# Performance work log

Hardware: AMD Instinct MI355X
Metric: run time of the kernel (lower is better)

Reference implementation:

```python
import jax, jax.numpy as jnp
import numpy as np
from jax.scipy.ndimage import map_coordinates


def _so3_exp(w):
    # Rodrigues formula, small-angle safe. w: [B,3] -> [B,3,3]
    th = jnp.linalg.norm(w, axis=-1)
    small = th < 1e-6
    ths = jnp.where(small, 1.0, th)
    A = jnp.where(small, 1.0 - th * th / 6.0, jnp.sin(ths) / ths)
    Bc = jnp.where(small, 0.5 - th * th / 24.0, (1.0 - jnp.cos(ths)) / (ths * ths))
    wx, wy, wz = w[..., 0], w[..., 1], w[..., 2]
    z = jnp.zeros_like(wx)
    K = jnp.stack([
        jnp.stack([z, -wz, wy], -1),
        jnp.stack([wz, z, -wx], -1),
        jnp.stack([-wy, wx, z], -1),
    ], -2)
    I = jnp.eye(3, dtype=w.dtype)
    return I + A[..., None, None] * K + Bc[..., None, None] * (K @ K)


def _pose(rot, xyz, rt_inv, isocenter):
    # pivot about isocenter expressed in camera frame (transform_point(rt_inv^-1, iso))
    iso_h = jnp.concatenate([isocenter, jnp.ones((1,), isocenter.dtype)])
    c = (jnp.linalg.inv(rt_inv[0]) @ iso_h)[:3]
    I4 = jnp.eye(4, dtype=rot.dtype)
    pivot = I4.at[:3, 3].set(c)
    pivot_inv = I4.at[:3, 3].set(-c)
    R = _so3_exp(rot)[0]
    t = R @ xyz[0]  # einsum('bij,bj->bi', R, xyz)
    T = I4.at[:3, :3].set(R).at[:3, 3].set(t)
    return pivot @ T @ pivot_inv


def _render(volume, k_inv, ext, sdd, height, width, n_samples):
    # DRR: cast one ray per detector pixel from the source, trilinearly sample
    # the CT volume at n_samples midpoints along source->target, accumulate.
    Rw = ext[:3, :3]
    src = ext[:3, 3]
    u = jnp.arange(width, dtype=volume.dtype) + 0.5
    v = jnp.arange(height, dtype=volume.dtype) + 0.5
    uu, vv = jnp.meshgrid(u, v, indexing='xy')  # [H,W]
    pix = jnp.stack([uu, vv, jnp.ones_like(uu)], -1)  # [H,W,3]
    dirs = jnp.einsum('ij,hwj->hwi', k_inv[0], pix)  # camera-frame ray dirs
    tgt = src + sdd[0] * jnp.einsum('ij,hwj->hwi', Rw, dirs)  # detector points in world
    seg = tgt - src  # [H,W,3]
    tvals = (jnp.arange(n_samples, dtype=volume.dtype) + 0.5) / n_samples
    pts = src + tvals[:, None, None, None] * seg[None]  # [n,H,W,3] (voxel coords)
    step = jnp.linalg.norm(seg, axis=-1) / n_samples  # [H,W] per-sample path length
    vals = map_coordinates(volume, [pts[..., 0], pts[..., 1], pts[..., 2]],
                           order=1, mode='constant', cval=0.0)  # [n,H,W]
    img = vals.sum(0) * step
    return img[None, None]  # [1,1,H,W]


def setup_inputs() -> dict:
    key = jax.random.key(0)
    k1, k2, k3 = jax.random.split(key, 3)
    D = 256
    volume = jax.random.uniform(k1, (D, D, D), dtype=jnp.float32)
    isocenter = jnp.array([128.0, 128.0, 128.0], jnp.float32)
    sdd = jnp.array([600.0], jnp.float32)
    f, cx, cy = 850.0, 256.0, 256.0
    K = jnp.array([[f, 0.0, cx], [0.0, f, cy], [0.0, 0.0, 1.0]], jnp.float32)
    k_inv = jnp.linalg.inv(K)[None]
    rt_inv = jnp.eye(4, dtype=jnp.float32).at[:3, 3].set(
        jnp.array([128.0, 128.0, -472.0], jnp.float32))[None]
    rot = 1e-8 * jax.random.normal(k2, (1, 3), jnp.float32)
    xyz = 1e-8 * jax.random.normal(k3, (1, 3), jnp.float32)
    return {"volume": volume, "isocenter": isocenter, "rt_inv": rt_inv,
            "k_inv": k_inv, "sdd": sdd, "rot": rot, "xyz": xyz,
            "height": 512, "width": 512, "n_samples": 128}


def reference(volume, isocenter, rt_inv, k_inv, sdd, rot, xyz, height, width, n_samples):
    pose = _pose(rot, xyz, rt_inv, isocenter)
    ext = rt_inv[0] @ pose  # rt_inv @ pose
    return _render(volume, k_inv, ext, sdd, height, width, n_samples)
```

## Files before the change

### kernel.cpp

```cpp
#include <hip/hip_runtime.h>
#include <math.h>

#define VD 256
#define PAIR_BYTES (VD * VD * VD * 4UL)

__device__ inline unsigned short f2bf(float f) {
    unsigned int u = __float_as_uint(f);
    u += 0x7FFFu + ((u >> 16) & 1u);
    return (unsigned short)(u >> 16);
}

__device__ inline void invert4x4(const float* m, float* inv) {
    inv[0]  =  m[5]*m[10]*m[15] - m[5]*m[11]*m[14] - m[9]*m[6]*m[15] + m[9]*m[7]*m[14] + m[13]*m[6]*m[11] - m[13]*m[7]*m[10];
    inv[4]  = -m[4]*m[10]*m[15] + m[4]*m[11]*m[14] + m[8]*m[6]*m[15] - m[8]*m[7]*m[14] - m[12]*m[6]*m[11] + m[12]*m[7]*m[10];
    inv[8]  =  m[4]*m[9]*m[15]  - m[4]*m[11]*m[13] - m[8]*m[5]*m[15] + m[8]*m[7]*m[13] + m[12]*m[5]*m[11] - m[12]*m[7]*m[9];
    inv[12] = -m[4]*m[9]*m[14]  + m[4]*m[10]*m[13] + m[8]*m[5]*m[14] - m[8]*m[6]*m[13] - m[12]*m[5]*m[10] + m[12]*m[6]*m[9];
    inv[1]  = -m[1]*m[10]*m[15] + m[1]*m[11]*m[14] + m[9]*m[2]*m[15] - m[9]*m[3]*m[14] - m[13]*m[2]*m[11] + m[13]*m[3]*m[10];
    inv[5]  =  m[0]*m[10]*m[15] - m[0]*m[11]*m[14] - m[8]*m[2]*m[15] + m[8]*m[3]*m[14] + m[12]*m[2]*m[11] - m[12]*m[3]*m[10];
    inv[9]  = -m[0]*m[9]*m[15]  + m[0]*m[11]*m[13] + m[8]*m[1]*m[15] - m[8]*m[3]*m[13] - m[12]*m[1]*m[11] + m[12]*m[3]*m[9];
    inv[13] =  m[0]*m[9]*m[14]  - m[0]*m[10]*m[13] - m[8]*m[1]*m[14] + m[8]*m[2]*m[13] + m[12]*m[1]*m[10] - m[12]*m[2]*m[9];
    inv[2]  =  m[1]*m[6]*m[15]  - m[1]*m[7]*m[14]  - m[5]*m[2]*m[15] + m[5]*m[3]*m[14] + m[13]*m[2]*m[7]  - m[13]*m[3]*m[6];
    inv[6]  = -m[0]*m[6]*m[15]  + m[0]*m[7]*m[14]  + m[4]*m[2]*m[15] - m[4]*m[3]*m[14] - m[12]*m[2]*m[7]  + m[12]*m[3]*m[6];
    inv[10] =  m[0]*m[5]*m[15]  - m[0]*m[7]*m[13]  - m[4]*m[1]*m[15] + m[4]*m[3]*m[13] + m[12]*m[1]*m[7]  - m[12]*m[3]*m[5];
    inv[14] = -m[0]*m[5]*m[14]  + m[0]*m[6]*m[13]  + m[4]*m[1]*m[14] - m[4]*m[2]*m[13] - m[12]*m[1]*m[6]  + m[12]*m[2]*m[5];
    inv[3]  = -m[1]*m[6]*m[11]  + m[1]*m[7]*m[10]  + m[5]*m[2]*m[11] - m[5]*m[3]*m[10] - m[9]*m[2]*m[7]   + m[9]*m[3]*m[6];
    inv[7]  =  m[0]*m[6]*m[11]  - m[0]*m[7]*m[10]  - m[4]*m[2]*m[11] + m[4]*m[3]*m[10] + m[8]*m[2]*m[7]   - m[8]*m[3]*m[6];
    inv[11] = -m[0]*m[5]*m[11]  + m[0]*m[7]*m[9]   + m[4]*m[1]*m[11] - m[4]*m[3]*m[9]  - m[8]*m[1]*m[7]   + m[8]*m[3]*m[5];
    inv[15] =  m[0]*m[5]*m[10]  - m[0]*m[6]*m[9]   - m[4]*m[1]*m[10] + m[4]*m[2]*m[9]  + m[8]*m[1]*m[6]   - m[8]*m[2]*m[5];
    float det = m[0]*inv[0] + m[1]*inv[4] + m[2]*inv[8] + m[3]*inv[12];
    float rdet = 1.0f / det;
    for (int i = 0; i < 16; i++) inv[i] *= rdet;
}

__device__ inline void compute_pose(const float* __restrict__ iso,
                                    const float* __restrict__ rt,
                                    const float* __restrict__ kinv,
                                    const float* __restrict__ sdd,
                                    const float* __restrict__ rot,
                                    const float* __restrict__ xyz,
                                    float* M, float* src3) {
    float m[16];
    for (int i = 0; i < 16; i++) m[i] = rt[i];
    float minv[16];
    invert4x4(m, minv);
    float c0 = minv[0]*iso[0] + minv[1]*iso[1] + minv[2]*iso[2]  + minv[3];
    float c1 = minv[4]*iso[0] + minv[5]*iso[1] + minv[6]*iso[2]  + minv[7];
    float c2 = minv[8]*iso[0] + minv[9]*iso[1] + minv[10]*iso[2] + minv[11];
    float wx = rot[0], wy = rot[1], wz = rot[2];
    float th2 = wx*wx + wy*wy + wz*wz;
    float th = sqrtf(th2);
    float Ac, Bc;
    if (th < 1e-6f) { Ac = 1.0f - th2 / 6.0f; Bc = 0.5f - th2 / 24.0f; }
    else            { Ac = sinf(th) / th;     Bc = (1.0f - cosf(th)) / th2; }
    float R[9];
    R[0] = 1.0f + Bc * (-(wy*wy + wz*wz));
    R[1] = Ac * (-wz) + Bc * (wx*wy);
    R[2] = Ac * ( wy) + Bc * (wx*wz);
    R[3] = Ac * ( wz) + Bc * (wx*wy);
    R[4] = 1.0f + Bc * (-(wx*wx + wz*wz));
    R[5] = Ac * (-wx) + Bc * (wy*wz);
    R[6] = Ac * (-wy) + Bc * (wx*wz);
    R[7] = Ac * ( wx) + Bc * (wy*wz);
    R[8] = 1.0f + Bc * (-(wx*wx + wy*wy));
    float tx = R[0]*xyz[0] + R[1]*xyz[1] + R[2]*xyz[2];
    float ty = R[3]*xyz[0] + R[4]*xyz[1] + R[5]*xyz[2];
    float tz = R[6]*xyz[0] + R[7]*xyz[1] + R[8]*xyz[2];
    float pt0 = c0 + tx - (R[0]*c0 + R[1]*c1 + R[2]*c2);
    float pt1 = c1 + ty - (R[3]*c0 + R[4]*c1 + R[5]*c2);
    float pt2 = c2 + tz - (R[6]*c0 + R[7]*c1 + R[8]*c2);
    float E[12];
    for (int i = 0; i < 3; i++) {
        for (int j = 0; j < 3; j++)
            E[i*4+j] = rt[i*4+0]*R[0*3+j] + rt[i*4+1]*R[1*3+j] + rt[i*4+2]*R[2*3+j];
        E[i*4+3] = rt[i*4+0]*pt0 + rt[i*4+1]*pt1 + rt[i*4+2]*pt2 + rt[i*4+3];
    }
    float s = sdd[0];
    for (int i = 0; i < 3; i++)
        for (int j = 0; j < 3; j++)
            M[i*3+j] = s * (E[i*4+0]*kinv[0*3+j] + E[i*4+1]*kinv[1*3+j] + E[i*4+2]*kinv[2*3+j]);
    src3[0] = E[3]; src3[1] = E[7]; src3[2] = E[11];
}

__global__ __launch_bounds__(256)
void transpose_k(const float* __restrict__ in, unsigned int* __restrict__ Tp,
                 const float* __restrict__ iso, const float* __restrict__ rt,
                 const float* __restrict__ kinv, const float* __restrict__ sdd,
                 const float* __restrict__ rot, const float* __restrict__ xyz,
                 const int* __restrict__ pH, const int* __restrict__ pW) {
    __shared__ int B[6];
    __shared__ unsigned short tile[32][72];
    const int t = threadIdx.x;
    if (t == 0) {
        float M[9], src3[3];
        compute_pose(iso, rt, kinv, sdd, rot, xyz, M, src3);
        float W = (float)pW[0], H = (float)pH[0];
        float us[2] = {0.5f, W - 0.5f};
        float vs[2] = {0.5f, H - 0.5f};
        for (int a = 0; a < 3; a++) {
            float gmin = 1e30f, gmax = -1e30f;
            for (int i = 0; i < 2; i++)
                for (int j = 0; j < 2; j++) {
                    float g = M[a*3+0]*us[i] + M[a*3+1]*vs[j] + M[a*3+2];
                    gmin = fminf(gmin, g); gmax = fmaxf(gmax, g);
                }
            float sa = src3[a];
            int loi = (int)floorf(sa + fminf(0.0f, gmin)) - 4;
            int hii = (int)ceilf (sa + fmaxf(0.0f, gmax)) + 5;
            B[2*a]   = min(max(loi, 0), VD - 1);
            B[2*a+1] = min(max(hii, 0), VD - 1);
        }
    }
    __syncthreads();
    const int x0 = blockIdx.x * 64;
    const int z0 = blockIdx.y * 32;
    const int y  = blockIdx.z;
    if (x0 + 63 < B[0] || x0 > B[1] || y < B[2] || y > B[3] ||
        z0 + 31 < B[4] || z0 > B[5]) return;

    {
        const int zq = t & 7;
        const int xl = t >> 3;
        #pragma unroll
        for (int i = 0; i < 2; i++) {
            int xr = xl + 32 * i;
            const float4 f = *(const float4*)(in + (((size_t)(x0 + xr)) << 16) + (y << 8) + z0 + 4*zq);
            tile[4*zq+0][xr] = f2bf(f.x);
            tile[4*zq+1][xr] = f2bf(f.y);
            tile[4*zq+2][xr] = f2bf(f.z);
            tile[4*zq+3][xr] = f2bf(f.w);
        }
        if (t < 8) {
            int xs = min(x0 + 64, VD - 1);
            const float4 f = *(const float4*)(in + (((size_t)xs) << 16) + (y << 8) + z0 + 4*t);
            tile[4*t+0][64] = f2bf(f.x);
            tile[4*t+1][64] = f2bf(f.y);
            tile[4*t+2][64] = f2bf(f.z);
            tile[4*t+3][64] = f2bf(f.w);
        }
    }
    __syncthreads();
    {
        const int xq = t & 15;
        const int zl = t >> 4;
        #pragma unroll
        for (int i = 0; i < 2; i++) {
            int zr = zl + 16 * i;
            const uint2 aa = *reinterpret_cast<const uint2*>(&tile[zr][4*xq]);
            unsigned int a0 = aa.x & 0xFFFFu, a1 = aa.x >> 16;
            unsigned int a2 = aa.y & 0xFFFFu, a3 = aa.y >> 16;
            unsigned int a4 = tile[zr][4*xq+4];
            uint4 o;
            o.x = a0 | (a1 << 16);
            o.y = a1 | (a2 << 16);
            o.z = a2 | (a3 << 16);
            o.w = a3 | (a4 << 16);
            *(uint4*)(Tp + (((size_t)(z0 + zr)) << 16) + (y << 8) + x0 + 4*xq) = o;
        }
    }
}

__device__ inline float sample_guarded(const unsigned int* __restrict__ Tp,
                                       float x, float y, float z) {
    float fx = floorf(x); int ix = (int)fx; float ax = x - fx;
    float fy = floorf(y); int iy = (int)fy; float ay = y - fy;
    float fz = floorf(z); int iz = (int)fz; float az = z - fz;

    float wx0v = ((unsigned)ix       < (unsigned)VD) ? (1.0f - ax) : 0.0f;
    float wx1v = ((unsigned)(ix + 1) < (unsigned)VD) ? ax : 0.0f;
    int bx = min(max(ix, 0), VD - 1);
    int sxi = ix - bx;
    float w0p = (sxi == 0) ? wx0v : ((sxi == -1) ? wx1v : 0.0f);
    float w1p = (sxi == 0) ? wx1v : 0.0f;

    float wy0 = ((unsigned)iy       < (unsigned)VD) ? (1.0f - ay) : 0.0f;
    float wy1 = ((unsigned)(iy + 1) < (unsigned)VD) ? ay : 0.0f;
    float wz0 = ((unsigned)iz       < (unsigned)VD) ? (1.0f - az) : 0.0f;
    float wz1 = ((unsigned)(iz + 1) < (unsigned)VD) ? az : 0.0f;

    int iy0 = min(max(iy, 0), VD - 1), iy1 = min(max(iy + 1, 0), VD - 1);
    int iz0 = min(max(iz, 0), VD - 1), iz1 = min(max(iz + 1, 0), VD - 1);

    int i00 = (iz0 << 16) + (iy0 << 8) + bx;
    int i01 = i00 + ((iy1 - iy0) << 8);
    int i10 = i00 + ((iz1 - iz0) << 16);
    int i11 = i10 + ((iy1 - iy0) << 8);

    unsigned int p00 = Tp[i00];
    unsigned int p01 = Tp[i01];
    unsigned int p10 = Tp[i10];
    unsigned int p11 = Tp[i11];

    float f00a = __uint_as_float(p00 << 16), f00b = __uint_as_float(p00 & 0xFFFF0000u);
    float f01a = __uint_as_float(p01 << 16), f01b = __uint_as_float(p01 & 0xFFFF0000u);
    float f10a = __uint_as_float(p10 << 16), f10b = __uint_as_float(p10 & 0xFFFF0000u);
    float f11a = __uint_as_float(p11 << 16), f11b = __uint_as_float(p11 & 0xFFFF0000u);

    float cx00 = fmaf(f00a, w0p, f00b * w1p);
    float cx01 = fmaf(f01a, w0p, f01b * w1p);
    float cx10 = fmaf(f10a, w0p, f10b * w1p);
    float cx11 = fmaf(f11a, w0p, f11b * w1p);

    float cy0 = fmaf(cx00, wy0, cx01 * wy1);
    float cy1 = fmaf(cx10, wy0, cx11 * wy1);
    return cy0 * wz0 + cy1 * wz1;
}

__global__ __launch_bounds__(256)
void render_pair(const unsigned int* __restrict__ Tp,
                 const float* __restrict__ iso, const float* __restrict__ rt,
                 const float* __restrict__ kinv, const float* __restrict__ sdd,
                 const float* __restrict__ rot, const float* __restrict__ xyz,
                 const int* __restrict__ pW, const int* __restrict__ pN,
                 float* __restrict__ out, int total) {
    __shared__ float S[12];
    if (threadIdx.x == 0) {
        float M[9], src3[3];
        compute_pose(iso, rt, kinv, sdd, rot, xyz, M, src3);
        for (int i = 0; i < 9; i++) S[i] = M[i];
        S[9] = src3[0]; S[10] = src3[1]; S[11] = src3[2];
    }
    __syncthreads();
    int tid = blockIdx.x * 256 + threadIdx.x;
    if (tid >= total) return;
    const int W = pW[0];
    const int N = pN[0];
    int w = tid % W;
    int h = tid / W;
    float u = (float)w + 0.5f;
    float v = (float)h + 0.5f;

    float gx = S[0]*u + S[1]*v + S[2];
    float gy = S[3]*u + S[4]*v + S[5];
    float gz = S[6]*u + S[7]*v + S[8];
    float sx = S[9], sy = S[10], sz = S[11];
    float len = sqrtf(gx*gx + gy*gy + gz*gz);
    float invN = 1.0f / (float)N;

    float t0 = 0.0f, t1 = 1.0f;
    float tA = 0.0f, tB = 1.0f;
    {
        const float HI = (float)(VD - 1) - 0.01f;
        float s3[3] = {sx, sy, sz};
        float g3[3] = {gx, gy, gz};
        for (int a = 0; a < 3; a++) {
            float g = g3[a], s = s3[a];
            if (fabsf(g) > 1e-20f) {
                float rg = 1.0f / g;
                float ta = (-1.0f - s) * rg;
                float tb = ((float)VD - s) * rg;
                t0 = fmaxf(t0, fminf(ta, tb));
                t1 = fminf(t1, fmaxf(ta, tb));
                float tc = (0.0f - s) * rg;
                float td = (HI - s) * rg;
                tA = fmaxf(tA, fminf(tc, td));
                tB = fminf(tB, fmaxf(tc, td));
            } else {
                if (s <= -1.0f || s >= (float)VD) t1 = -1.0f;
                if (s < 0.0f || s > HI)           tB = -2.0f;
            }
        }
    }
    int k0 = (int)floorf(t0 * (float)N - 0.5f) - 1;
    int k1 = (int)ceilf (t1 * (float)N - 0.5f) + 1;
    if (k0 < 0) k0 = 0;
    if (k1 > N - 1) k1 = N - 1;
    int kA = (int)ceilf (tA * (float)N - 0.5f) + 1;
    int kB = (int)floorf(tB * (float)N - 0.5f) - 1;
    kA = max(kA, k0);
    kB = min(kB, k1);

    float acc = 0.0f;
    int headEnd = min(kA - 1, k1);
    for (int k = k0; k <= headEnd; k++) {
        float t = ((float)k + 0.5f) * invN;
        acc += sample_guarded(Tp, fmaf(t, gx, sx), fmaf(t, gy, sy), fmaf(t, gz, sz));
    }
    #pragma unroll 2
    for (int k = kA; k <= kB; k++) {
        float t = ((float)k + 0.5f) * invN;
        float x = fmaf(t, gx, sx);
        float y = fmaf(t, gy, sy);
        float z = fmaf(t, gz, sz);
        float fx = floorf(x); int ix = (int)fx; float ax = x - fx;
        float fy = floorf(y); int iy = (int)fy; float ay = y - fy;
        float fz = floorf(z); int iz = (int)fz; float az = z - fz;
        int idx = (iz << 16) + (iy << 8) + ix;
        unsigned int p00 = Tp[idx];
        unsigned int p01 = Tp[idx + 256];
        unsigned int p10 = Tp[idx + 65536];
        unsigned int p11 = Tp[idx + 65536 + 256];
        float f00a = __uint_as_float(p00 << 16), f00b = __uint_as_float(p00 & 0xFFFF0000u);
        float f01a = __uint_as_float(p01 << 16), f01b = __uint_as_float(p01 & 0xFFFF0000u);
        float f10a = __uint_as_float(p10 << 16), f10b = __uint_as_float(p10 & 0xFFFF0000u);
        float f11a = __uint_as_float(p11 << 16), f11b = __uint_as_float(p11 & 0xFFFF0000u);
        float cx00 = fmaf(f00b - f00a, ax, f00a);
        float cx01 = fmaf(f01b - f01a, ax, f01a);
        float cx10 = fmaf(f10b - f10a, ax, f10a);
        float cx11 = fmaf(f11b - f11a, ax, f11a);
        float cy0 = fmaf(cx01 - cx00, ay, cx00);
        float cy1 = fmaf(cx11 - cx10, ay, cx10);
        acc += fmaf(cy1 - cy0, az, cy0);
    }
    int tailStart = max(kB + 1, kA);
    for (int k = tailStart; k <= k1; k++) {
        float t = ((float)k + 0.5f) * invN;
        acc += sample_guarded(Tp, fmaf(t, gx, sx), fmaf(t, gy, sy), fmaf(t, gz, sz));
    }
    out[tid] = acc * len * invN;
}

__global__ __launch_bounds__(256)
void render_direct(const float* __restrict__ vol,
                   const float* __restrict__ iso, const float* __restrict__ rt,
                   const float* __restrict__ kinv, const float* __restrict__ sdd,
                   const float* __restrict__ rot, const float* __restrict__ xyz,
                   const int* __restrict__ pW, const int* __restrict__ pN,
                   float* __restrict__ out, int total) {
    __shared__ float S[12];
    if (threadIdx.x == 0) {
        float M[9], src3[3];
        compute_pose(iso, rt, kinv, sdd, rot, xyz, M, src3);
        for (int i = 0; i < 9; i++) S[i] = M[i];
        S[9] = src3[0]; S[10] = src3[1]; S[11] = src3[2];
    }
    __syncthreads();
    int tid = blockIdx.x * 256 + threadIdx.x;
    if (tid >= total) return;
    const int W = pW[0];
    const int N = pN[0];
    int w = tid % W;
    int h = tid / W;
    float u = (float)w + 0.5f;
    float v = (float)h + 0.5f;
    float gx = S[0]*u + S[1]*v + S[2];
    float gy = S[3]*u + S[4]*v + S[5];
    float gz = S[6]*u + S[7]*v + S[8];
    float sx = S[9], sy = S[10], sz = S[11];
    float len = sqrtf(gx*gx + gy*gy + gz*gz);
    float invN = 1.0f / (float)N;
    float acc = 0.0f;
    for (int k = 0; k < N; k++) {
        float t = ((float)k + 0.5f) * invN;
        float x = fmaf(t, gx, sx);
        float y = fmaf(t, gy, sy);
        float z = fmaf(t, gz, sz);
        float fx = floorf(x); int ix = (int)fx; float ax = x - fx;
        float fy = floorf(y); int iy = (int)fy; float ay = y - fy;
        float fz = floorf(z); int iz = (int)fz; float az = z - fz;
        float wx0 = ((unsigned)ix       < (unsigned)VD) ? (1.0f - ax) : 0.0f;
        float wx1 = ((unsigned)(ix + 1) < (unsigned)VD) ? ax : 0.0f;
        float wy0 = ((unsigned)iy       < (unsigned)VD) ? (1.0f - ay) : 0.0f;
        float wy1 = ((unsigned)(iy + 1) < (unsigned)VD) ? ay : 0.0f;
        float wz0 = ((unsigned)iz       < (unsigned)VD) ? (1.0f - az) : 0.0f;
        float wz1 = ((unsigned)(iz + 1) < (unsigned)VD) ? az : 0.0f;
        int ix0 = min(max(ix, 0), VD - 1), ix1 = min(max(ix + 1, 0), VD - 1);
        int iy0 = min(max(iy, 0), VD - 1), iy1 = min(max(iy + 1, 0), VD - 1);
        int iz0 = min(max(iz, 0), VD - 1), iz1 = min(max(iz + 1, 0), VD - 1);
        int X0 = ix0 << 16, X1 = ix1 << 16;
        int Y0 = iy0 << 8,  Y1 = iy1 << 8;
        float v000 = vol[X0 + Y0 + iz0];
        float v001 = vol[X0 + Y0 + iz1];
        float v010 = vol[X0 + Y1 + iz0];
        float v011 = vol[X0 + Y1 + iz1];
        float v100 = vol[X1 + Y0 + iz0];
        float v101 = vol[X1 + Y0 + iz1];
        float v110 = vol[X1 + Y1 + iz0];
        float v111 = vol[X1 + Y1 + iz1];
        float c00 = fmaf(v000, wz0, v001 * wz1);
        float c01 = fmaf(v010, wz0, v011 * wz1);
        float c10 = fmaf(v100, wz0, v101 * wz1);
        float c11 = fmaf(v110, wz0, v111 * wz1);
        float c0  = fmaf(c00, wy0, c01 * wy1);
        float c1  = fmaf(c10, wy0, c11 * wy1);
        acc += fmaf(c0, wx0, c1 * wx1);
    }
    out[tid] = acc * len * invN;
}

extern "C" void kernel_launch(void* const* d_in, const int* in_sizes, int n_in,
                              void* d_out, int out_size, void* d_ws, size_t ws_size,
                              hipStream_t stream) {
    const float* vol  = (const float*)d_in[0];
    const float* iso  = (const float*)d_in[1];
    const float* rt   = (const float*)d_in[2];
    const float* kinv = (const float*)d_in[3];
    const float* sdd  = (const float*)d_in[4];
    const float* rot  = (const float*)d_in[5];
    const float* xyz  = (const float*)d_in[6];
    const int* pH = (const int*)d_in[7];
    const int* pW = (const int*)d_in[8];
    const int* pN = (const int*)d_in[9];
    float* out = (float*)d_out;
    int total = out_size;

    if (ws_size >= PAIR_BYTES) {
        unsigned int* Tp = (unsigned int*)d_ws;
        transpose_k<<<dim3(4, 8, 256), 256, 0, stream>>>(vol, Tp, iso, rt, kinv, sdd, rot, xyz, pH, pW);
        render_pair<<<(total + 255) / 256, 256, 0, stream>>>(Tp, iso, rt, kinv, sdd, rot, xyz, pW, pN, out, total);
    } else {
        render_direct<<<(total + 255) / 256, 256, 0, stream>>>(vol, iso, rt, kinv, sdd, rot, xyz, pW, pN, out, total);
    }
}
```

Measured before the change: 143.4 us.

## Switch paired volume storage to fp16 and interpolate with packed half2 math

Converts the pre-transposed paired volume from bf16 to fp16 and does the y/z trilinear lerps in the interior loop with packed half2 FMAs, leaving only the x lerp in fp32. It also replaces per-sample position recomputation with incremental stepping and truncation instead of floorf. The goal is fewer ALU instructions per sample in the hot loop. In exchange it adds fp16 rounding of weights and intermediates and accumulates drift in positions from repeated addition, which can shift sample indices near voxel boundaries.

```diff
diff --git a/kernel.cpp b/kernel.cpp
--- a/kernel.cpp
+++ b/kernel.cpp
@@ -1,13 +1,12 @@
 #include <hip/hip_runtime.h>
+#include <hip/hip_fp16.h>
 #include <math.h>
 
 #define VD 256
 #define PAIR_BYTES (VD * VD * VD * 4UL)
 
-__device__ inline unsigned short f2bf(float f) {
-    unsigned int u = __float_as_uint(f);
-    u += 0x7FFFu + ((u >> 16) & 1u);
-    return (unsigned short)(u >> 16);
+__device__ inline __half2 u2h2(unsigned int p) {
+    return *reinterpret_cast<__half2*>(&p);
 }
 
 __device__ inline void invert4x4(const float* m, float* inv) {
@@ -124,18 +123,22 @@
         for (int i = 0; i < 2; i++) {
             int xr = xl + 32 * i;
             const float4 f = *(const float4*)(in + (((size_t)(x0 + xr)) << 16) + (y << 8) + z0 + 4*zq);
-            tile[4*zq+0][xr] = f2bf(f.x);
-            tile[4*zq+1][xr] = f2bf(f.y);
-            tile[4*zq+2][xr] = f2bf(f.z);
-            tile[4*zq+3][xr] = f2bf(f.w);
+            __half2 h01 = __float22half2_rn(make_float2(f.x, f.y));
+            __half2 h23 = __float22half2_rn(make_float2(f.z, f.w));
+            tile[4*zq+0][xr] = __half_as_ushort(__low2half(h01));
+            tile[4*zq+1][xr] = __half_as_ushort(__high2half(h01));
+            tile[4*zq+2][xr] = __half_as_ushort(__low2half(h23));
+            tile[4*zq+3][xr] = __half_as_ushort(__high2half(h23));
         }
         if (t < 8) {
             int xs = min(x0 + 64, VD - 1);
             const float4 f = *(const float4*)(in + (((size_t)xs) << 16) + (y << 8) + z0 + 4*t);
-            tile[4*t+0][64] = f2bf(f.x);
-            tile[4*t+1][64] = f2bf(f.y);
-            tile[4*t+2][64] = f2bf(f.z);
-            tile[4*t+3][64] = f2bf(f.w);
+            __half2 h01 = __float22half2_rn(make_float2(f.x, f.y));
+            __half2 h23 = __float22half2_rn(make_float2(f.z, f.w));
+            tile[4*t+0][64] = __half_as_ushort(__low2half(h01));
+            tile[4*t+1][64] = __half_as_ushort(__high2half(h01));
+            tile[4*t+2][64] = __half_as_ushort(__low2half(h23));
+            tile[4*t+3][64] = __half_as_ushort(__high2half(h23));
         }
     }
     __syncthreads();
@@ -146,14 +149,12 @@
         for (int i = 0; i < 2; i++) {
             int zr = zl + 16 * i;
             const uint2 aa = *reinterpret_cast<const uint2*>(&tile[zr][4*xq]);
-            unsigned int a0 = aa.x & 0xFFFFu, a1 = aa.x >> 16;
-            unsigned int a2 = aa.y & 0xFFFFu, a3 = aa.y >> 16;
-            unsigned int a4 = tile[zr][4*xq+4];
+            unsigned int h4 = tile[zr][4*xq+4];
             uint4 o;
-            o.x = a0 | (a1 << 16);
-            o.y = a1 | (a2 << 16);
-            o.z = a2 | (a3 << 16);
-            o.w = a3 | (a4 << 16);
+            o.x = aa.x;
+            o.y = (aa.x >> 16) | (aa.y << 16);
+            o.z = aa.y;
+            o.w = (aa.y >> 16) | (h4 << 16);
             *(uint4*)(Tp + (((size_t)(z0 + zr)) << 16) + (y << 8) + x0 + 4*xq) = o;
         }
     }
@@ -185,15 +186,14 @@
     int i10 = i00 + ((iz1 - iz0) << 16);
     int i11 = i10 + ((iy1 - iy0) << 8);
 
-    unsigned int p00 = Tp[i00];
-    unsigned int p01 = Tp[i01];
-    unsigned int p10 = Tp[i10];
-    unsigned int p11 = Tp[i11];
-
-    float f00a = __uint_as_float(p00 << 16), f00b = __uint_as_float(p00 & 0xFFFF0000u);
-    float f01a = __uint_as_float(p01 << 16), f01b = __uint_as_float(p01 & 0xFFFF0000u);
-    float f10a = __uint_as_float(p10 << 16), f10b = __uint_as_float(p10 & 0xFFFF0000u);
-    float f11a = __uint_as_float(p11 << 16), f11b = __uint_as_float(p11 & 0xFFFF0000u);
+    __half2 h00 = u2h2(Tp[i00]);
+    __half2 h01 = u2h2(Tp[i01]);
+    __half2 h10 = u2h2(Tp[i10]);
+    __half2 h11 = u2h2(Tp[i11]);
+    float f00a = __low2float(h00), f00b = __high2float(h00);
+    float f01a = __low2float(h01), f01b = __high2float(h01);
+    float f10a = __low2float(h10), f10b = __high2float(h10);
+    float f11a = __low2float(h11), f11b = __high2float(h11);
 
     float cx00 = fmaf(f00a, w0p, f00b * w1p);
     float cx01 = fmaf(f01a, w0p, f01b * w1p);
@@ -275,31 +275,35 @@
         float t = ((float)k + 0.5f) * invN;
         acc += sample_guarded(Tp, fmaf(t, gx, sx), fmaf(t, gy, sy), fmaf(t, gz, sz));
     }
-    #pragma unroll 2
-    for (int k = kA; k <= kB; k++) {
-        float t = ((float)k + 0.5f) * invN;
-        float x = fmaf(t, gx, sx);
-        float y = fmaf(t, gy, sy);
-        float z = fmaf(t, gz, sz);
-        float fx = floorf(x); int ix = (int)fx; float ax = x - fx;
-        float fy = floorf(y); int iy = (int)fy; float ay = y - fy;
-        float fz = floorf(z); int iz = (int)fz; float az = z - fz;
-        int idx = (iz << 16) + (iy << 8) + ix;
-        unsigned int p00 = Tp[idx];
-        unsigned int p01 = Tp[idx + 256];
-        unsigned int p10 = Tp[idx + 65536];
-        unsigned int p11 = Tp[idx + 65536 + 256];
-        float f00a = __uint_as_float(p00 << 16), f00b = __uint_as_float(p00 & 0xFFFF0000u);
-        float f01a = __uint_as_float(p01 << 16), f01b = __uint_as_float(p01 & 0xFFFF0000u);
-        float f10a = __uint_as_float(p10 << 16), f10b = __uint_as_float(p10 & 0xFFFF0000u);
-        float f11a = __uint_as_float(p11 << 16), f11b = __uint_as_float(p11 & 0xFFFF0000u);
-        float cx00 = fmaf(f00b - f00a, ax, f00a);
-        float cx01 = fmaf(f01b - f01a, ax, f01a);
-        float cx10 = fmaf(f10b - f10a, ax, f10a);
-        float cx11 = fmaf(f11b - f11a, ax, f11a);
-        float cy0 = fmaf(cx01 - cx00, ay, cx00);
-        float cy1 = fmaf(cx11 - cx10, ay, cx10);
-        acc += fmaf(cy1 - cy0, az, cy0);
+    if (kA <= kB) {
+        float dx = gx * invN, dy = gy * invN, dz = gz * invN;
+        float tS = ((float)kA + 0.5f) * invN;
+        float x = fmaf(tS, gx, sx);
+        float y = fmaf(tS, gy, sy);
+        float z = fmaf(tS, gz, sz);
+        #pragma unroll 2
+        for (int k = kA; k <= kB; k++) {
+            int ix = (int)x; float ax = x - (float)ix;
+            int iy = (int)y; float ay = y - (float)iy;
+            int iz = (int)z; float az = z - (float)iz;
+            int idx = (iz << 16) + (iy << 8) + ix;
+            unsigned int p00 = Tp[idx];
+            unsigned int p01 = Tp[idx + 256];
+            unsigned int p10 = Tp[idx + 65536];
+            unsigned int p11 = Tp[idx + 65536 + 256];
+            __half2 h00 = u2h2(p00);
+            __half2 h01 = u2h2(p01);
+            __half2 h10 = u2h2(p10);
+            __half2 h11 = u2h2(p11);
+            __half2 ay2 = __float2half2_rn(ay);
+            __half2 az2 = __float2half2_rn(az);
+            __half2 cy0 = __hfma2(__hsub2(h01, h00), ay2, h00);
+            __half2 cy1 = __hfma2(__hsub2(h11, h10), ay2, h10);
+            __half2 cz  = __hfma2(__hsub2(cy1, cy0), az2, cy0);
+            float a = __low2float(cz), b = __high2float(cz);
+            acc += fmaf(b - a, ax, a);
+            x += dx; y += dy; z += dz;
+        }
     }
     int tailStart = max(kB + 1, kA);
     for (int k = tailStart; k <= k1; k++) {
```

New measurement: 146.1 us. About the same (+1.9%).
